# Optimization experiments

Measured on AMD Instinct MI355X. Metric: run time of the kernel, lower is better.

The kernel has to match this reference:

```python
import jax, jax.numpy as jnp
import numpy as np

SCALE = 0.08838834764831845  # 1/sqrt(head_size=128)
NEG_INF = -1e9


def setup_inputs() -> dict:
    key = jax.random.key(0)
    ks = jax.random.split(key, 8)
    NH, HS = 32, 128                 # heads, head_size
    NP, NS, G = 2048, 4, 64          # prompt tokens, prompt seqs, decode tokens
    NT = NP + G                      # total valid tokens
    NB, BS, MB = 1024, 16, 32        # num cache blocks, block_size, max blocks/seq
    q = jax.random.normal(ks[0], (NT, NH * HS), jnp.float32)
    k = jax.random.normal(ks[1], (NT, NH * HS), jnp.float32)
    v = jax.random.normal(ks[2], (NT, NH * HS), jnp.float32)
    kc = jax.random.normal(ks[3], (NB, NH, HS, BS), jnp.float32)
    vc = jax.random.normal(ks[4], (NB, NH, HS, BS), jnp.float32)
    bt = jax.random.randint(ks[5], (G, MB), 0, NB, jnp.int32)
    cl = jax.random.randint(ks[6], (G,), 1, MB * BS + 1, jnp.int32)  # >=1 so softmax is defined
    sm = jax.random.randint(ks[7], (NT,), 0, NB * BS, jnp.int32)
    return {"query": q, "key": k, "value": v, "key_cache": kc, "value_cache": vc,
            "block_tables": bt, "context_lens": cl, "slot_mapping": sm,
            "num_prompt_tokens": NP, "num_prompt_seqs": NS}


def reference(query, key, value, key_cache, value_cache, block_tables,
              context_lens, slot_mapping, num_prompt_tokens, num_prompt_seqs):
    NB, NH, HS, BS = key_cache.shape
    q = query.reshape(-1, NH, HS)
    k = key.reshape(-1, NH, HS)
    v = value.reshape(-1, NH, HS)
    NP, NS = num_prompt_tokens, num_prompt_seqs
    L = NP // NS  # equal-length prompts -> block-diagonal causal == batched causal

    # --- prompt phase: multi-query causal MHA (xformers path) ---
    qp = q[:NP].reshape(NS, L, NH, HS)
    kp = k[:NP].reshape(NS, L, NH, HS)
    vp = v[:NP].reshape(NS, L, NH, HS)
    scores = jnp.einsum('bqhd,bkhd->bhqk', qp, kp) * SCALE
    causal = jnp.tril(jnp.ones((L, L), bool))
    scores = jnp.where(causal, scores, NEG_INF)
    probs = jax.nn.softmax(scores, axis=-1)
    out_p = jnp.einsum('bhqk,bkhd->bqhd', probs, vp).reshape(NP, NH, HS)

    # --- reshape_and_cache: scatter all valid tokens' K/V into paged cache ---
    blk = slot_mapping // BS
    off = slot_mapping % BS
    key_cache = key_cache.at[blk, :, :, off].set(k)
    value_cache = value_cache.at[blk, :, :, off].set(v)

    # --- decode phase: single-query paged attention over block tables ---
    qd = q[NP:]                                  # [G, NH, HS]
    G, MB = block_tables.shape
    # gather blocks: [G, MB, NH, HS, BS] -> [G, MB*BS, NH, HS]
    kd = jnp.transpose(key_cache[block_tables], (0, 1, 4, 2, 3)).reshape(G, MB * BS, NH, HS)
    vd = jnp.transpose(value_cache[block_tables], (0, 1, 4, 2, 3)).reshape(G, MB * BS, NH, HS)
    sc = jnp.einsum('ghd,gkhd->ghk', qd, kd) * SCALE
    valid = jnp.arange(MB * BS)[None, :] < context_lens[:, None]   # [G, K]
    sc = jnp.where(valid[:, None, :], sc, NEG_INF)
    pd = jax.nn.softmax(sc, axis=-1)
    out_d = jnp.einsum('ghk,gkhd->ghd', pd, vd)

    out = jnp.concatenate([out_p, out_d], axis=0)
    return out.reshape(-1, NH * HS)
```

## Files before the change

### kernel.cpp

```cpp
#include <hip/hip_runtime.h>
#include <stdint.h>

#define NH    32
#define HS    128
#define NPT   2048
#define NT    2112
#define NBLK  1024
#define BS    16
#define MBMAX 32
#define LSEQ  512
#define DMODEL 4096
#define SCALE 0.08838834764831845f

typedef __bf16 bf16x8 __attribute__((ext_vector_type(8)));
typedef float  f32x4  __attribute__((ext_vector_type(4)));

__device__ __forceinline__ unsigned short f2bf(float f) {
    unsigned u = __float_as_uint(f);
    u += 0x7fffu + ((u >> 16) & 1u);
    return (unsigned short)(u >> 16);
}
__device__ __forceinline__ unsigned pack2(float a, float b) {
    return (unsigned)f2bf(a) | ((unsigned)f2bf(b) << 16);
}
__device__ __forceinline__ float sel4(const float a[4], int i) {
    float r = a[0];
    r = (i == 1) ? a[1] : r;
    r = (i == 2) ? a[2] : r;
    r = (i == 3) ? a[3] : r;
    return r;
}

__global__ void fill_winner(const int* __restrict__ sm, int* __restrict__ w) {
    int t = blockIdx.x * 256 + threadIdx.x;
    if (t < NT) atomicMax(&w[sm[t]], t);
}

#define QKS 136
__device__ __forceinline__ int vtidx(int d, int t) {
    return d * 72 + (t ^ (((d >> 3) & 3) * 8));
}

__global__ __launch_bounds__(256, 2) void prompt_attn(
    const float* __restrict__ q, const float* __restrict__ k,
    const float* __restrict__ v, float* __restrict__ out) {

    __shared__ __align__(16) unsigned short Ks[64 * QKS];
    __shared__ __align__(16) unsigned short Vt[128 * 72 + 32];
    __shared__ __align__(16) unsigned short Ps[4 * 16 * 72];

    const int tid  = threadIdx.x;
    const int lane = tid & 63, wq = tid >> 6;
    const int quad = lane >> 4, m15 = lane & 15;
    const int qt = 7 - (blockIdx.x & 7);
    const int h  = (blockIdx.x >> 3) & 31;
    const int s  = blockIdx.x >> 8;
    const int qbase  = s * LSEQ + qt * 64;
    const int kbase0 = s * LSEQ;

    bf16x8 aq[4];
    {
        const float* qr = q + (size_t)(qbase + wq * 16 + m15) * DMODEL + h * HS + quad * 8;
        #pragma unroll
        for (int kc = 0; kc < 4; ++kc) {
            float4 t0 = *(const float4*)(qr + kc * 32);
            float4 t1 = *(const float4*)(qr + kc * 32 + 4);
            union { unsigned u[4]; bf16x8 v; } cv;
            cv.u[0] = pack2(t0.x * SCALE, t0.y * SCALE);
            cv.u[1] = pack2(t0.z * SCALE, t0.w * SCALE);
            cv.u[2] = pack2(t1.x * SCALE, t1.y * SCALE);
            cv.u[3] = pack2(t1.z * SCALE, t1.w * SCALE);
            aq[kc] = cv.v;
        }
    }

    f32x4 O[8];
    #pragma unroll
    for (int i = 0; i < 8; ++i) O[i] = (f32x4){0.f, 0.f, 0.f, 0.f};
    float mrun[4], lrun[4];
    #pragma unroll
    for (int r = 0; r < 4; ++r) { mrun[r] = -1e30f; lrun[r] = 0.f; }

    unsigned short* Pw = Ps + wq * (16 * 72);

    const int r0 = tid >> 5, c4 = (tid & 31) * 4;
    const int gv = tid >> 2, sub = tid & 3;
    const int lbase = lane & ~3;

    float4 kreg[8], vreg[8];
    #pragma unroll
    for (int p = 0; p < 8; ++p) {
        int r = r0 + p * 8;
        kreg[p] = *(const float4*)(k + (size_t)(kbase0 + r) * DMODEL + h * HS + c4);
    }
    #pragma unroll
    for (int p = 0; p < 8; ++p) {
        const int tb = (p & 3) * 16, db = (p >> 2) * 64;
        const int tok  = tb + (gv >> 4) * 4 + sub;
        const int dim4 = db + (gv & 15) * 4;
        vreg[p] = *(const float4*)(v + (size_t)(kbase0 + tok) * DMODEL + h * HS + dim4);
    }

    for (int kt = 0; kt <= qt; ++kt) {
        #pragma unroll
        for (int p = 0; p < 8; ++p) {
            int r = r0 + p * 8;
            float4 t = kreg[p];
            uint2 w; w.x = pack2(t.x, t.y); w.y = pack2(t.z, t.w);
            *(uint2*)(&Ks[r * QKS + c4]) = w;
        }
        #pragma unroll
        for (int p = 0; p < 8; ++p) {
            const int tb = (p & 3) * 16, db = (p >> 2) * 64;
            const int dim4 = db + (gv & 15) * 4;
            float4 t = vreg[p];
            float in[4] = {t.x, t.y, t.z, t.w};
            float rec[4];
            #pragma unroll
            for (int r = 0; r < 4; ++r) {
                float pub = sel4(in, (sub + 4 - r) & 3);
                rec[r] = __shfl(pub, lbase + ((sub + r) & 3));
            }
            float o4[4];
            #pragma unroll
            for (int j = 0; j < 4; ++j) o4[j] = sel4(rec, (j + 4 - sub) & 3);
            const int d  = dim4 + sub;
            const int t0 = tb + (gv >> 4) * 4;
            uint2 w2; w2.x = pack2(o4[0], o4[1]); w2.y = pack2(o4[2], o4[3]);
            *(uint2*)(&Vt[vtidx(d, t0)]) = w2;
        }
        __syncthreads();

        if (kt < qt) {
            #pragma unroll
            for (int p = 0; p < 8; ++p) {
                int r = r0 + p * 8;
                kreg[p] = *(const float4*)(k + (size_t)(kbase0 + (kt + 1) * 64 + r) * DMODEL + h * HS + c4);
            }
            #pragma unroll
            for (int p = 0; p < 8; ++p) {
                const int tb = (p & 3) * 16, db = (p >> 2) * 64;
                const int tok  = tb + (gv >> 4) * 4 + sub;
                const int dim4 = db + (gv & 15) * 4;
                vreg[p] = *(const float4*)(v + (size_t)(kbase0 + (kt + 1) * 64 + tok) * DMODEL + h * HS + dim4);
            }
        }

        f32x4 S[4];
        #pragma unroll
        for (int nt = 0; nt < 4; ++nt) {
            S[nt] = (f32x4){0.f, 0.f, 0.f, 0.f};
            #pragma unroll
            for (int kc = 0; kc < 4; ++kc) {
                bf16x8 bk = *(const bf16x8*)(&Ks[(nt * 16 + m15) * QKS + kc * 32 + quad * 8]);
                S[nt] = __builtin_amdgcn_mfma_f32_16x16x32_bf16(aq[kc], bk, S[nt], 0, 0, 0);
            }
        }
        if (kt == qt) {
            #pragma unroll
            for (int nt = 0; nt < 4; ++nt) {
                const int C = nt * 16 + m15;
                #pragma unroll
                for (int reg = 0; reg < 4; ++reg) {
                    const int R = wq * 16 + quad * 4 + reg;
                    if (C > R) S[nt][reg] = -1e30f;
                }
            }
        }

        #pragma unroll
        for (int reg = 0; reg < 4; ++reg) {
            float x = fmaxf(fmaxf(S[0][reg], S[1][reg]), fmaxf(S[2][reg], S[3][reg]));
            x = fmaxf(x, __shfl_xor(x, 1));
            x = fmaxf(x, __shfl_xor(x, 2));
            x = fmaxf(x, __shfl_xor(x, 4));
            x = fmaxf(x, __shfl_xor(x, 8));
            const float mn = fmaxf(mrun[reg], x);
            const float al = __expf(mrun[reg] - mn);
            mrun[reg] = mn;
            float sum = 0.f;
            #pragma unroll
            for (int nt = 0; nt < 4; ++nt) {
                float pv = __expf(S[nt][reg] - mn);
                S[nt][reg] = pv;
                sum += pv;
            }
            sum += __shfl_xor(sum, 1);
            sum += __shfl_xor(sum, 2);
            sum += __shfl_xor(sum, 4);
            sum += __shfl_xor(sum, 8);
            lrun[reg] = lrun[reg] * al + sum;
            #pragma unroll
            for (int n2 = 0; n2 < 8; ++n2) O[n2][reg] *= al;
        }

        #pragma unroll
        for (int nt = 0; nt < 4; ++nt) {
            #pragma unroll
            for (int reg = 0; reg < 4; ++reg) {
                float v0 = S[nt][reg];
                float v1 = __shfl_xor(v0, 1);
                if (!(lane & 1))
                    *(unsigned*)(&Pw[(quad * 4 + reg) * 72 + nt * 16 + m15]) = pack2(v0, v1);
            }
        }

        bf16x8 ap[2];
        #pragma unroll
        for (int kc = 0; kc < 2; ++kc)
            ap[kc] = *(const bf16x8*)(&Pw[m15 * 72 + kc * 32 + quad * 8]);
        #pragma unroll
        for (int n2 = 0; n2 < 8; ++n2) {
            #pragma unroll
            for (int kc = 0; kc < 2; ++kc) {
                bf16x8 bv = *(const bf16x8*)(&Vt[vtidx(n2 * 16 + m15, kc * 32 + quad * 8)]);
                O[n2] = __builtin_amdgcn_mfma_f32_16x16x32_bf16(ap[kc], bv, O[n2], 0, 0, 0);
            }
        }
        __syncthreads();
    }

    float inv[4];
    #pragma unroll
    for (int reg = 0; reg < 4; ++reg) inv[reg] = 1.f / lrun[reg];
    #pragma unroll
    for (int n2 = 0; n2 < 8; ++n2) {
        #pragma unroll
        for (int reg = 0; reg < 4; ++reg) {
            out[(size_t)(qbase + wq * 16 + quad * 4 + reg) * DMODEL + h * HS + n2 * 16 + m15] =
                O[n2][reg] * inv[reg];
        }
    }
}

__global__ __launch_bounds__(256, 3) void decode_attn(
    const float* __restrict__ q, const float* __restrict__ k, const float* __restrict__ v,
    const float* __restrict__ kcache, const float* __restrict__ vcache,
    const int* __restrict__ bt, const int* __restrict__ cl,
    const int* __restrict__ winner, float* __restrict__ out) {

    __shared__ float pm[4], pl[4];
    __shared__ float pacc[4][128];

    const int tid = threadIdx.x, w = tid >> 6, lane = tid & 63;
    const int g = blockIdx.x >> 5, h = blockIdx.x & 31;
    const int n  = cl[g];
    const int nb = (n + 15) >> 4;

    const int p4 = lane >> 2;
    const int ob = (lane & 3) * 4;

    const float* qp = q + (size_t)(NPT + g) * DMODEL + h * HS;
    float qreg[8];
    #pragma unroll
    for (int i = 0; i < 8; ++i) qreg[i] = qp[p4 + 16 * i] * SCALE;

    float m = -1e30f, l = 0.f;
    float acc[8];
    #pragma unroll
    for (int i = 0; i < 8; ++i) acc[i] = 0.f;

    f32x4 kv[8], vv[8];
    int blk = 0;
    if (w < nb) {
        blk = bt[g * MBMAX + w];
        const float* kb = kcache + ((size_t)blk * NH + h) * (HS * BS);
        #pragma unroll
        for (int i = 0; i < 8; ++i)
            kv[i] = *(const f32x4*)(kb + lane * 4 + i * 256);
    }

    for (int jb = w; jb < nb; jb += 4) {
        const float* vb = vcache + ((size_t)blk * NH + h) * (HS * BS);
        #pragma unroll
        for (int i = 0; i < 8; ++i)
            vv[i] = *(const f32x4*)(vb + lane * 4 + i * 256);

        const int4 wt4 = *(const int4*)(winner + blk * BS + ob);
        const int wtj[4] = {wt4.x, wt4.y, wt4.z, wt4.w};
        const bool anyw = __any(wt4.x >= 0 || wt4.y >= 0 || wt4.z >= 0 || wt4.w >= 0);

        if (anyw) {
            #pragma unroll
            for (int j = 0; j < 4; ++j) {
                if (wtj[j] >= 0) {
                    const float* fr = k + (size_t)wtj[j] * DMODEL + h * HS + p4;
                    #pragma unroll
                    for (int i = 0; i < 8; ++i) kv[i][j] = fr[16 * i];
                }
            }
        }

        float s[4];
        #pragma unroll
        for (int j = 0; j < 4; ++j) s[j] = 0.f;
        #pragma unroll
        for (int i = 0; i < 8; ++i) {
            s[0] += qreg[i] * kv[i][0];
            s[1] += qreg[i] * kv[i][1];
            s[2] += qreg[i] * kv[i][2];
            s[3] += qreg[i] * kv[i][3];
        }
        #pragma unroll
        for (int j = 0; j < 4; ++j) {
            s[j] += __shfl_xor(s[j], 4);
            s[j] += __shfl_xor(s[j], 8);
            s[j] += __shfl_xor(s[j], 16);
            s[j] += __shfl_xor(s[j], 32);
            if (jb * 16 + ob + j >= n) s[j] = -1e30f;
        }

        float tm = fmaxf(fmaxf(s[0], s[1]), fmaxf(s[2], s[3]));
        tm = fmaxf(tm, __shfl_xor(tm, 1));
        tm = fmaxf(tm, __shfl_xor(tm, 2));
        const float mn = fmaxf(m, tm);
        const float al = __expf(m - mn);
        m = mn;
        float p[4], ps = 0.f;
        #pragma unroll
        for (int j = 0; j < 4; ++j) { p[j] = __expf(s[j] - mn); ps += p[j]; }
        ps += __shfl_xor(ps, 1);
        ps += __shfl_xor(ps, 2);
        l = l * al + ps;
        #pragma unroll
        for (int i = 0; i < 8; ++i) acc[i] *= al;

        const int jn = jb + 4;
        if (jn < nb) {
            blk = bt[g * MBMAX + jn];
            const float* kb = kcache + ((size_t)blk * NH + h) * (HS * BS);
            #pragma unroll
            for (int i = 0; i < 8; ++i)
                kv[i] = *(const f32x4*)(kb + lane * 4 + i * 256);
        }

        if (anyw) {
            #pragma unroll
            for (int j = 0; j < 4; ++j) {
                if (wtj[j] >= 0) {
                    const float* fr = v + (size_t)wtj[j] * DMODEL + h * HS + p4;
                    #pragma unroll
                    for (int i = 0; i < 8; ++i) vv[i][j] = fr[16 * i];
                }
            }
        }
        #pragma unroll
        for (int i = 0; i < 8; ++i)
            acc[i] += p[0] * vv[i][0] + p[1] * vv[i][1]
                    + p[2] * vv[i][2] + p[3] * vv[i][3];
    }

    #pragma unroll
    for (int i = 0; i < 8; ++i) {
        acc[i] += __shfl_xor(acc[i], 1);
        acc[i] += __shfl_xor(acc[i], 2);
    }
    if (lane == 0) { pm[w] = m; pl[w] = l; }
    if ((lane & 3) == 0) {
        #pragma unroll
        for (int i = 0; i < 8; ++i) pacc[w][p4 + 16 * i] = acc[i];
    }
    __syncthreads();
    if (tid < 128) {
        const float M = fmaxf(fmaxf(pm[0], pm[1]), fmaxf(pm[2], pm[3]));
        float L = 0.f, A = 0.f;
        #pragma unroll
        for (int w2 = 0; w2 < 4; ++w2) {
            const float e = __expf(pm[w2] - M);
            L += e * pl[w2];
            A += e * pacc[w2][tid];
        }
        out[(size_t)(NPT + g) * DMODEL + h * HS + tid] = A / L;
    }
}

extern "C" void kernel_launch(void* const* d_in, const int* in_sizes, int n_in,
                              void* d_out, int out_size, void* d_ws, size_t ws_size,
                              hipStream_t stream) {
    const float* q  = (const float*)d_in[0];
    const float* k  = (const float*)d_in[1];
    const float* v  = (const float*)d_in[2];
    const float* kc = (const float*)d_in[3];
    const float* vc = (const float*)d_in[4];
    const int* bt   = (const int*)d_in[5];
    const int* cl   = (const int*)d_in[6];
    const int* sm   = (const int*)d_in[7];
    float* out  = (float*)d_out;
    int* winner = (int*)d_ws;

    hipMemsetAsync(winner, 0xFF, (size_t)NBLK * BS * sizeof(int), stream);
    hipLaunchKernelGGL(fill_winner, dim3(9),    dim3(256), 0, stream, sm, winner);
    hipLaunchKernelGGL(prompt_attn, dim3(1024), dim3(256), 0, stream, q, k, v, out);
    hipLaunchKernelGGL(decode_attn, dim3(2048), dim3(256), 0, stream,
                       q, k, v, kc, vc, bt, cl, winner, out);
}
```

Measured before the change: 708.8 us.

## Fuse prompt and decode attention into one interleaved launch

Merges the prompt flash-attention kernel and the paged decode kernel into a single launch of 3072 blocks. Every third block runs a prompt tile and the other two run decode (group, head) pairs, so the two workloads run side by side on the GPU instead of one after the other. The prompt path also drops its register prefetch of the next K/V tile and loads directly before the LDS store, which cuts register use so the fused kernel can keep its 3-blocks-per-SM launch bound, at the cost of exposing load latency. Shared memory per block becomes the sum of both paths, which may limit occupancy.

```diff
diff --git a/kernel.cpp b/kernel.cpp
--- a/kernel.cpp
+++ b/kernel.cpp
@@ -41,336 +41,310 @@
     return d * 72 + (t ^ (((d >> 3) & 3) * 8));
 }
 
-__global__ __launch_bounds__(256, 2) void prompt_attn(
-    const float* __restrict__ q, const float* __restrict__ k,
-    const float* __restrict__ v, float* __restrict__ out) {
+__global__ __launch_bounds__(256, 3) void fused_attn(
+    const float* __restrict__ q, const float* __restrict__ k, const float* __restrict__ v,
+    const float* __restrict__ kcache, const float* __restrict__ vcache,
+    const int* __restrict__ bt, const int* __restrict__ cl,
+    const int* __restrict__ winner, float* __restrict__ out) {
 
     __shared__ __align__(16) unsigned short Ks[64 * QKS];
     __shared__ __align__(16) unsigned short Vt[128 * 72 + 32];
     __shared__ __align__(16) unsigned short Ps[4 * 16 * 72];
+    __shared__ float pm[4], pl[4];
+    __shared__ float pacc[4][128];
 
     const int tid  = threadIdx.x;
-    const int lane = tid & 63, wq = tid >> 6;
-    const int quad = lane >> 4, m15 = lane & 15;
-    const int qt = 7 - (blockIdx.x & 7);
-    const int h  = (blockIdx.x >> 3) & 31;
-    const int s  = blockIdx.x >> 8;
-    const int qbase  = s * LSEQ + qt * 64;
-    const int kbase0 = s * LSEQ;
-
-    bf16x8 aq[4];
-    {
-        const float* qr = q + (size_t)(qbase + wq * 16 + m15) * DMODEL + h * HS + quad * 8;
-        #pragma unroll
-        for (int kc = 0; kc < 4; ++kc) {
-            float4 t0 = *(const float4*)(qr + kc * 32);
-            float4 t1 = *(const float4*)(qr + kc * 32 + 4);
-            union { unsigned u[4]; bf16x8 v; } cv;
-            cv.u[0] = pack2(t0.x * SCALE, t0.y * SCALE);
-            cv.u[1] = pack2(t0.z * SCALE, t0.w * SCALE);
-            cv.u[2] = pack2(t1.x * SCALE, t1.y * SCALE);
-            cv.u[3] = pack2(t1.z * SCALE, t1.w * SCALE);
-            aq[kc] = cv.v;
-        }
-    }
-
-    f32x4 O[8];
-    #pragma unroll
-    for (int i = 0; i < 8; ++i) O[i] = (f32x4){0.f, 0.f, 0.f, 0.f};
-    float mrun[4], lrun[4];
-    #pragma unroll
-    for (int r = 0; r < 4; ++r) { mrun[r] = -1e30f; lrun[r] = 0.f; }
-
-    unsigned short* Pw = Ps + wq * (16 * 72);
-
-    const int r0 = tid >> 5, c4 = (tid & 31) * 4;
-    const int gv = tid >> 2, sub = tid & 3;
-    const int lbase = lane & ~3;
-
-    float4 kreg[8], vreg[8];
-    #pragma unroll
-    for (int p = 0; p < 8; ++p) {
-        int r = r0 + p * 8;
-        kreg[p] = *(const float4*)(k + (size_t)(kbase0 + r) * DMODEL + h * HS + c4);
-    }
-    #pragma unroll
-    for (int p = 0; p < 8; ++p) {
-        const int tb = (p & 3) * 16, db = (p >> 2) * 64;
-        const int tok  = tb + (gv >> 4) * 4 + sub;
-        const int dim4 = db + (gv & 15) * 4;
-        vreg[p] = *(const float4*)(v + (size_t)(kbase0 + tok) * DMODEL + h * HS + dim4);
-    }
-
-    for (int kt = 0; kt <= qt; ++kt) {
-        #pragma unroll
-        for (int p = 0; p < 8; ++p) {
-            int r = r0 + p * 8;
-            float4 t = kreg[p];
-            uint2 w; w.x = pack2(t.x, t.y); w.y = pack2(t.z, t.w);
-            *(uint2*)(&Ks[r * QKS + c4]) = w;
-        }
-        #pragma unroll
-        for (int p = 0; p < 8; ++p) {
-            const int tb = (p & 3) * 16, db = (p >> 2) * 64;
-            const int dim4 = db + (gv & 15) * 4;
-            float4 t = vreg[p];
-            float in[4] = {t.x, t.y, t.z, t.w};
-            float rec[4];
-            #pragma unroll
-            for (int r = 0; r < 4; ++r) {
-                float pub = sel4(in, (sub + 4 - r) & 3);
-                rec[r] = __shfl(pub, lbase + ((sub + r) & 3));
-            }
-            float o4[4];
-            #pragma unroll
-            for (int j = 0; j < 4; ++j) o4[j] = sel4(rec, (j + 4 - sub) & 3);
-            const int d  = dim4 + sub;
-            const int t0 = tb + (gv >> 4) * 4;
-            uint2 w2; w2.x = pack2(o4[0], o4[1]); w2.y = pack2(o4[2], o4[3]);
-            *(uint2*)(&Vt[vtidx(d, t0)]) = w2;
-        }
-        __syncthreads();
-
-        if (kt < qt) {
+    const int lane = tid & 63;
+    const int bid  = blockIdx.x;
+    const int rr   = bid % 3;
+    const int bb   = bid / 3;
+
+    if (rr == 0) {
+        const int wq = tid >> 6;
+        const int quad = lane >> 4, m15 = lane & 15;
+        const int qt = 7 - (bb & 7);
+        const int h  = (bb >> 3) & 31;
+        const int s  = bb >> 8;
+        const int qbase  = s * LSEQ + qt * 64;
+        const int kbase0 = s * LSEQ;
+
+        bf16x8 aq[4];
+        {
+            const float* qr = q + (size_t)(qbase + wq * 16 + m15) * DMODEL + h * HS + quad * 8;
+            #pragma unroll
+            for (int kc = 0; kc < 4; ++kc) {
+                float4 t0 = *(const float4*)(qr + kc * 32);
+                float4 t1 = *(const float4*)(qr + kc * 32 + 4);
+                union { unsigned u[4]; bf16x8 v; } cv;
+                cv.u[0] = pack2(t0.x * SCALE, t0.y * SCALE);
+                cv.u[1] = pack2(t0.z * SCALE, t0.w * SCALE);
+                cv.u[2] = pack2(t1.x * SCALE, t1.y * SCALE);
+                cv.u[3] = pack2(t1.z * SCALE, t1.w * SCALE);
+                aq[kc] = cv.v;
+            }
+        }
+
+        f32x4 O[8];
+        #pragma unroll
+        for (int i = 0; i < 8; ++i) O[i] = (f32x4){0.f, 0.f, 0.f, 0.f};
+        float mrun[4], lrun[4];
+        #pragma unroll
+        for (int r = 0; r < 4; ++r) { mrun[r] = -1e30f; lrun[r] = 0.f; }
+
+        unsigned short* Pw = Ps + wq * (16 * 72);
+
+        const int r0 = tid >> 5, c4 = (tid & 31) * 4;
+        const int gv = tid >> 2, sub = tid & 3;
+        const int lbase = lane & ~3;
+
+        for (int kt = 0; kt <= qt; ++kt) {
             #pragma unroll
             for (int p = 0; p < 8; ++p) {
                 int r = r0 + p * 8;
-                kreg[p] = *(const float4*)(k + (size_t)(kbase0 + (kt + 1) * 64 + r) * DMODEL + h * HS + c4);
+                float4 t = *(const float4*)(k + (size_t)(kbase0 + kt * 64 + r) * DMODEL + h * HS + c4);
+                uint2 w; w.x = pack2(t.x, t.y); w.y = pack2(t.z, t.w);
+                *(uint2*)(&Ks[r * QKS + c4]) = w;
             }
             #pragma unroll
             for (int p = 0; p < 8; ++p) {
                 const int tb = (p & 3) * 16, db = (p >> 2) * 64;
                 const int tok  = tb + (gv >> 4) * 4 + sub;
                 const int dim4 = db + (gv & 15) * 4;
-                vreg[p] = *(const float4*)(v + (size_t)(kbase0 + (kt + 1) * 64 + tok) * DMODEL + h * HS + dim4);
-            }
-        }
-
-        f32x4 S[4];
-        #pragma unroll
-        for (int nt = 0; nt < 4; ++nt) {
-            S[nt] = (f32x4){0.f, 0.f, 0.f, 0.f};
-            #pragma unroll
-            for (int kc = 0; kc < 4; ++kc) {
-                bf16x8 bk = *(const bf16x8*)(&Ks[(nt * 16 + m15) * QKS + kc * 32 + quad * 8]);
-                S[nt] = __builtin_amdgcn_mfma_f32_16x16x32_bf16(aq[kc], bk, S[nt], 0, 0, 0);
-            }
-        }
-        if (kt == qt) {
+                float4 t = *(const float4*)(v + (size_t)(kbase0 + kt * 64 + tok) * DMODEL + h * HS + dim4);
+                float in[4] = {t.x, t.y, t.z, t.w};
+                float rec[4];
+                #pragma unroll
+                for (int r = 0; r < 4; ++r) {
+                    float pub = sel4(in, (sub + 4 - r) & 3);
+                    rec[r] = __shfl(pub, lbase + ((sub + r) & 3));
+                }
+                float o4[4];
+                #pragma unroll
+                for (int j = 0; j < 4; ++j) o4[j] = sel4(rec, (j + 4 - sub) & 3);
+                const int d  = dim4 + sub;
+                const int t0 = tb + (gv >> 4) * 4;
+                uint2 w2; w2.x = pack2(o4[0], o4[1]); w2.y = pack2(o4[2], o4[3]);
+                *(uint2*)(&Vt[vtidx(d, t0)]) = w2;
+            }
+            __syncthreads();
+
+            f32x4 S[4];
             #pragma unroll
             for (int nt = 0; nt < 4; ++nt) {
-                const int C = nt * 16 + m15;
+                S[nt] = (f32x4){0.f, 0.f, 0.f, 0.f};
+                #pragma unroll
+                for (int kc = 0; kc < 4; ++kc) {
+                    bf16x8 bk = *(const bf16x8*)(&Ks[(nt * 16 + m15) * QKS + kc * 32 + quad * 8]);
+                    S[nt] = __builtin_amdgcn_mfma_f32_16x16x32_bf16(aq[kc], bk, S[nt], 0, 0, 0);
+                }
+            }
+            if (kt == qt) {
+                #pragma unroll
+                for (int nt = 0; nt < 4; ++nt) {
+                    const int C = nt * 16 + m15;
+                    #pragma unroll
+                    for (int reg = 0; reg < 4; ++reg) {
+                        const int R = wq * 16 + quad * 4 + reg;
+                        if (C > R) S[nt][reg] = -1e30f;
+                    }
+                }
+            }
+
+            #pragma unroll
+            for (int reg = 0; reg < 4; ++reg) {
+                float x = fmaxf(fmaxf(S[0][reg], S[1][reg]), fmaxf(S[2][reg], S[3][reg]));
+                x = fmaxf(x, __shfl_xor(x, 1));
+                x = fmaxf(x, __shfl_xor(x, 2));
+                x = fmaxf(x, __shfl_xor(x, 4));
+                x = fmaxf(x, __shfl_xor(x, 8));
+                const float mn = fmaxf(mrun[reg], x);
+                const float al = __expf(mrun[reg] - mn);
+                mrun[reg] = mn;
+                float sum = 0.f;
+                #pragma unroll
+                for (int nt = 0; nt < 4; ++nt) {
+                    float pv = __expf(S[nt][reg] - mn);
+                    S[nt][reg] = pv;
+                    sum += pv;
+                }
+                sum += __shfl_xor(sum, 1);
+                sum += __shfl_xor(sum, 2);
+                sum += __shfl_xor(sum, 4);
+                sum += __shfl_xor(sum, 8);
+                lrun[reg] = lrun[reg] * al + sum;
+                #pragma unroll
+                for (int n2 = 0; n2 < 8; ++n2) O[n2][reg] *= al;
+            }
+
+            #pragma unroll
+            for (int nt = 0; nt < 4; ++nt) {
                 #pragma unroll
                 for (int reg = 0; reg < 4; ++reg) {
-                    const int R = wq * 16 + quad * 4 + reg;
-                    if (C > R) S[nt][reg] = -1e30f;
-                }
-            }
-        }
-
-        #pragma unroll
-        for (int reg = 0; reg < 4; ++reg) {
-            float x = fmaxf(fmaxf(S[0][reg], S[1][reg]), fmaxf(S[2][reg], S[3][reg]));
-            x = fmaxf(x, __shfl_xor(x, 1));
-            x = fmaxf(x, __shfl_xor(x, 2));
-            x = fmaxf(x, __shfl_xor(x, 4));
-            x = fmaxf(x, __shfl_xor(x, 8));
-            const float mn = fmaxf(mrun[reg], x);
-            const float al = __expf(mrun[reg] - mn);
-            mrun[reg] = mn;
-            float sum = 0.f;
-            #pragma unroll
-            for (int nt = 0; nt < 4; ++nt) {
-                float pv = __expf(S[nt][reg] - mn);
-                S[nt][reg] = pv;
-                sum += pv;
-            }
-            sum += __shfl_xor(sum, 1);
-            sum += __shfl_xor(sum, 2);
-            sum += __shfl_xor(sum, 4);
-            sum += __shfl_xor(sum, 8);
-            lrun[reg] = lrun[reg] * al + sum;
-            #pragma unroll
-            for (int n2 = 0; n2 < 8; ++n2) O[n2][reg] *= al;
-        }
-
-        #pragma unroll
-        for (int nt = 0; nt < 4; ++nt) {
+                    float v0 = S[nt][reg];
+                    float v1 = __shfl_xor(v0, 1);
+                    if (!(lane & 1))
+                        *(unsigned*)(&Pw[(quad * 4 + reg) * 72 + nt * 16 + m15]) = pack2(v0, v1);
+                }
+            }
+
+            bf16x8 ap[2];
+            #pragma unroll
+            for (int kc = 0; kc < 2; ++kc)
+                ap[kc] = *(const bf16x8*)(&Pw[m15 * 72 + kc * 32 + quad * 8]);
+            #pragma unroll
+            for (int n2 = 0; n2 < 8; ++n2) {
+                #pragma unroll
+                for (int kc = 0; kc < 2; ++kc) {
+                    bf16x8 bv = *(const bf16x8*)(&Vt[vtidx(n2 * 16 + m15, kc * 32 + quad * 8)]);
+                    O[n2] = __builtin_amdgcn_mfma_f32_16x16x32_bf16(ap[kc], bv, O[n2], 0, 0, 0);
+                }
+            }
+            __syncthreads();
+        }
+
+        float inv[4];
+        #pragma unroll
+        for (int reg = 0; reg < 4; ++reg) inv[reg] = 1.f / lrun[reg];
+        #pragma unroll
+        for (int n2 = 0; n2 < 8; ++n2) {
             #pragma unroll
             for (int reg = 0; reg < 4; ++reg) {
-                float v0 = S[nt][reg];
-                float v1 = __shfl_xor(v0, 1);
-                if (!(lane & 1))
-                    *(unsigned*)(&Pw[(quad * 4 + reg) * 72 + nt * 16 + m15]) = pack2(v0, v1);
-            }
-        }
-
-        bf16x8 ap[2];
-        #pragma unroll
-        for (int kc = 0; kc < 2; ++kc)
-            ap[kc] = *(const bf16x8*)(&Pw[m15 * 72 + kc * 32 + quad * 8]);
-        #pragma unroll
-        for (int n2 = 0; n2 < 8; ++n2) {
-            #pragma unroll
-            for (int kc = 0; kc < 2; ++kc) {
-                bf16x8 bv = *(const bf16x8*)(&Vt[vtidx(n2 * 16 + m15, kc * 32 + quad * 8)]);
-                O[n2] = __builtin_amdgcn_mfma_f32_16x16x32_bf16(ap[kc], bv, O[n2], 0, 0, 0);
-            }
-        }
-        __syncthreads();
-    }
-
-    float inv[4];
-    #pragma unroll
-    for (int reg = 0; reg < 4; ++reg) inv[reg] = 1.f / lrun[reg];
-    #pragma unroll
-    for (int n2 = 0; n2 < 8; ++n2) {
-        #pragma unroll
-        for (int reg = 0; reg < 4; ++reg) {
-            out[(size_t)(qbase + wq * 16 + quad * 4 + reg) * DMODEL + h * HS + n2 * 16 + m15] =
-                O[n2][reg] * inv[reg];
-        }
-    }
-}
-
-__global__ __launch_bounds__(256, 3) void decode_attn(
-    const float* __restrict__ q, const float* __restrict__ k, const float* __restrict__ v,
-    const float* __restrict__ kcache, const float* __restrict__ vcache,
-    const int* __restrict__ bt, const int* __restrict__ cl,
-    const int* __restrict__ winner, float* __restrict__ out) {
-
-    __shared__ float pm[4], pl[4];
-    __shared__ float pacc[4][128];
-
-    const int tid = threadIdx.x, w = tid >> 6, lane = tid & 63;
-    const int g = blockIdx.x >> 5, h = blockIdx.x & 31;
-    const int n  = cl[g];
-    const int nb = (n + 15) >> 4;
-
-    const int p4 = lane >> 2;
-    const int ob = (lane & 3) * 4;
-
-    const float* qp = q + (size_t)(NPT + g) * DMODEL + h * HS;
-    float qreg[8];
-    #pragma unroll
-    for (int i = 0; i < 8; ++i) qreg[i] = qp[p4 + 16 * i] * SCALE;
-
-    float m = -1e30f, l = 0.f;
-    float acc[8];
-    #pragma unroll
-    for (int i = 0; i < 8; ++i) acc[i] = 0.f;
-
-    f32x4 kv[8], vv[8];
-    int blk = 0;
-    if (w < nb) {
-        blk = bt[g * MBMAX + w];
-        const float* kb = kcache + ((size_t)blk * NH + h) * (HS * BS);
-        #pragma unroll
-        for (int i = 0; i < 8; ++i)
-            kv[i] = *(const f32x4*)(kb + lane * 4 + i * 256);
-    }
-
-    for (int jb = w; jb < nb; jb += 4) {
-        const float* vb = vcache + ((size_t)blk * NH + h) * (HS * BS);
-        #pragma unroll
-        for (int i = 0; i < 8; ++i)
-            vv[i] = *(const f32x4*)(vb + lane * 4 + i * 256);
-
-        const int4 wt4 = *(const int4*)(winner + blk * BS + ob);
-        const int wtj[4] = {wt4.x, wt4.y, wt4.z, wt4.w};
-        const bool anyw = __any(wt4.x >= 0 || wt4.y >= 0 || wt4.z >= 0 || wt4.w >= 0);
-
-        if (anyw) {
-            #pragma unroll
-            for (int j = 0; j < 4; ++j) {
-                if (wtj[j] >= 0) {
-                    const float* fr = k + (size_t)wtj[j] * DMODEL + h * HS + p4;
-                    #pragma unroll
-                    for (int i = 0; i < 8; ++i) kv[i][j] = fr[16 * i];
-                }
-            }
-        }
-
-        float s[4];
-        #pragma unroll
-        for (int j = 0; j < 4; ++j) s[j] = 0.f;
-        #pragma unroll
-        for (int i = 0; i < 8; ++i) {
-            s[0] += qreg[i] * kv[i][0];
-            s[1] += qreg[i] * kv[i][1];
-            s[2] += qreg[i] * kv[i][2];
-            s[3] += qreg[i] * kv[i][3];
-        }
-        #pragma unroll
-        for (int j = 0; j < 4; ++j) {
-            s[j] += __shfl_xor(s[j], 4);
-            s[j] += __shfl_xor(s[j], 8);
-            s[j] += __shfl_xor(s[j], 16);
-            s[j] += __shfl_xor(s[j], 32);
-            if (jb * 16 + ob + j >= n) s[j] = -1e30f;
-        }
-
-        float tm = fmaxf(fmaxf(s[0], s[1]), fmaxf(s[2], s[3]));
-        tm = fmaxf(tm, __shfl_xor(tm, 1));
-        tm = fmaxf(tm, __shfl_xor(tm, 2));
-        const float mn = fmaxf(m, tm);
-        const float al = __expf(m - mn);
-        m = mn;
-        float p[4], ps = 0.f;
-        #pragma unroll
-        for (int j = 0; j < 4; ++j) { p[j] = __expf(s[j] - mn); ps += p[j]; }
-        ps += __shfl_xor(ps, 1);
-        ps += __shfl_xor(ps, 2);
-        l = l * al + ps;
-        #pragma unroll
-        for (int i = 0; i < 8; ++i) acc[i] *= al;
-
-        const int jn = jb + 4;
-        if (jn < nb) {
-            blk = bt[g * MBMAX + jn];
+                out[(size_t)(qbase + wq * 16 + quad * 4 + reg) * DMODEL + h * HS + n2 * 16 + m15] =
+                    O[n2][reg] * inv[reg];
+            }
+        }
+    } else {
+        const int dbid = bb * 2 + (rr - 1);
+        const int w = tid >> 6;
+        const int g = dbid >> 5, h = dbid & 31;
+        const int n  = cl[g];
+        const int nb = (n + 15) >> 4;
+
+        const int p4 = lane >> 2;
+        const int ob = (lane & 3) * 4;
+
+        const float* qp = q + (size_t)(NPT + g) * DMODEL + h * HS;
+        float qreg[8];
+        #pragma unroll
+        for (int i = 0; i < 8; ++i) qreg[i] = qp[p4 + 16 * i] * SCALE;
+
+        float m = -1e30f, l = 0.f;
+        float acc[8];
+        #pragma unroll
+        for (int i = 0; i < 8; ++i) acc[i] = 0.f;
+
+        f32x4 kv[8], vv[8];
+        int blk = 0;
+        if (w < nb) {
+            blk = bt[g * MBMAX + w];
             const float* kb = kcache + ((size_t)blk * NH + h) * (HS * BS);
             #pragma unroll
             for (int i = 0; i < 8; ++i)
                 kv[i] = *(const f32x4*)(kb + lane * 4 + i * 256);
         }
 
-        if (anyw) {
+        for (int jb = w; jb < nb; jb += 4) {
+            const float* vb = vcache + ((size_t)blk * NH + h) * (HS * BS);
+            #pragma unroll
+            for (int i = 0; i < 8; ++i)
+                vv[i] = *(const f32x4*)(vb + lane * 4 + i * 256);
+
+            const int4 wt4 = *(const int4*)(winner + blk * BS + ob);
+            const int wtj[4] = {wt4.x, wt4.y, wt4.z, wt4.w};
+            const bool anyw = __any(wt4.x >= 0 || wt4.y >= 0 || wt4.z >= 0 || wt4.w >= 0);
+
+            if (anyw) {
+                #pragma unroll
+                for (int j = 0; j < 4; ++j) {
+                    if (wtj[j] >= 0) {
+                        const float* fr = k + (size_t)wtj[j] * DMODEL + h * HS + p4;
+                        #pragma unroll
+                        for (int i = 0; i < 8; ++i) kv[i][j] = fr[16 * i];
+                    }
+                }
+            }
+
+            float s[4];
+            #pragma unroll
+            for (int j = 0; j < 4; ++j) s[j] = 0.f;
+            #pragma unroll
+            for (int i = 0; i < 8; ++i) {
+                s[0] += qreg[i] * kv[i][0];
+                s[1] += qreg[i] * kv[i][1];
+                s[2] += qreg[i] * kv[i][2];
+                s[3] += qreg[i] * kv[i][3];
+            }
             #pragma unroll
             for (int j = 0; j < 4; ++j) {
-                if (wtj[j] >= 0) {
-                    const float* fr = v + (size_t)wtj[j] * DMODEL + h * HS + p4;
-                    #pragma unroll
-                    for (int i = 0; i < 8; ++i) vv[i][j] = fr[16 * i];
-                }
-            }
-        }
-        #pragma unroll
-        for (int i = 0; i < 8; ++i)
-            acc[i] += p[0] * vv[i][0] + p[1] * vv[i][1]
-                    + p[2] * vv[i][2] + p[3] * vv[i][3];
-    }
-
-    #pragma unroll
-    for (int i = 0; i < 8; ++i) {
-        acc[i] += __shfl_xor(acc[i], 1);
-        acc[i] += __shfl_xor(acc[i], 2);
-    }
-    if (lane == 0) { pm[w] = m; pl[w] = l; }
-    if ((lane & 3) == 0) {
-        #pragma unroll
-        for (int i = 0; i < 8; ++i) pacc[w][p4 + 16 * i] = acc[i];
-    }
-    __syncthreads();
-    if (tid < 128) {
-        const float M = fmaxf(fmaxf(pm[0], pm[1]), fmaxf(pm[2], pm[3]));
-        float L = 0.f, A = 0.f;
-        #pragma unroll
-        for (int w2 = 0; w2 < 4; ++w2) {
-            const float e = __expf(pm[w2] - M);
-            L += e * pl[w2];
-            A += e * pacc[w2][tid];
-        }
-        out[(size_t)(NPT + g) * DMODEL + h * HS + tid] = A / L;
+                s[j] += __shfl_xor(s[j], 4);
+                s[j] += __shfl_xor(s[j], 8);
+                s[j] += __shfl_xor(s[j], 16);
+                s[j] += __shfl_xor(s[j], 32);
+                if (jb * 16 + ob + j >= n) s[j] = -1e30f;
+            }
+
+            float tm = fmaxf(fmaxf(s[0], s[1]), fmaxf(s[2], s[3]));
+            tm = fmaxf(tm, __shfl_xor(tm, 1));
+            tm = fmaxf(tm, __shfl_xor(tm, 2));
+            const float mn = fmaxf(m, tm);
+            const float al = __expf(m - mn);
+            m = mn;
+            float p[4], ps = 0.f;
+            #pragma unroll
+            for (int j = 0; j < 4; ++j) { p[j] = __expf(s[j] - mn); ps += p[j]; }
+            ps += __shfl_xor(ps, 1);
+            ps += __shfl_xor(ps, 2);
+            l = l * al + ps;
+            #pragma unroll
+            for (int i = 0; i < 8; ++i) acc[i] *= al;
+
+            const int jn = jb + 4;
+            if (jn < nb) {
+                blk = bt[g * MBMAX + jn];
+                const float* kb = kcache + ((size_t)blk * NH + h) * (HS * BS);
+                #pragma unroll
+                for (int i = 0; i < 8; ++i)
+                    kv[i] = *(const f32x4*)(kb + lane * 4 + i * 256);
+            }
+
+            if (anyw) {
+                #pragma unroll
+                for (int j = 0; j < 4; ++j) {
+                    if (wtj[j] >= 0) {
+                        const float* fr = v + (size_t)wtj[j] * DMODEL + h * HS + p4;
+                        #pragma unroll
+                        for (int i = 0; i < 8; ++i) vv[i][j] = fr[16 * i];
+                    }
+                }
+            }
+            #pragma unroll
+            for (int i = 0; i < 8; ++i)
+                acc[i] += p[0] * vv[i][0] + p[1] * vv[i][1]
+                        + p[2] * vv[i][2] + p[3] * vv[i][3];
+        }
+
+        #pragma unroll
+        for (int i = 0; i < 8; ++i) {
+            acc[i] += __shfl_xor(acc[i], 1);
+            acc[i] += __shfl_xor(acc[i], 2);
+        }
+        if (lane == 0) { pm[w] = m; pl[w] = l; }
+        if ((lane & 3) == 0) {
+            #pragma unroll
+            for (int i = 0; i < 8; ++i) pacc[w][p4 + 16 * i] = acc[i];
+        }
+        __syncthreads();
+        if (tid < 128) {
+            const float M = fmaxf(fmaxf(pm[0], pm[1]), fmaxf(pm[2], pm[3]));
+            float L = 0.f, A = 0.f;
+            #pragma unroll
+            for (int w2 = 0; w2 < 4; ++w2) {
+                const float e = __expf(pm[w2] - M);
+                L += e * pl[w2];
+                A += e * pacc[w2][tid];
+            }
+            out[(size_t)(NPT + g) * DMODEL + h * HS + tid] = A / L;
+        }
     }
 }
 
@@ -390,7 +364,6 @@
 
     hipMemsetAsync(winner, 0xFF, (size_t)NBLK * BS * sizeof(int), stream);
     hipLaunchKernelGGL(fill_winner, dim3(9),    dim3(256), 0, stream, sm, winner);
-    hipLaunchKernelGGL(prompt_attn, dim3(1024), dim3(256), 0, stream, q, k, v, out);
-    hipLaunchKernelGGL(decode_attn, dim3(2048), dim3(256), 0, stream,
+    hipLaunchKernelGGL(fused_attn,  dim3(3072), dim3(256), 0, stream,
                        q, k, v, kc, vc, bt, cl, winner, out);
 }
```

New measurement: 668.8 us. 1.06x faster.
